# Kernel tuning notes

Measured on AMD Instinct MI355X. Metric: run time of the kernel, lower is better.

The kernel has to match this reference:

```python
import jax, jax.numpy as jnp
import numpy as np

N = 200000   # gaussians
M = 10000    # scaffold nodes
K = 16       # skinning knn
T = 40       # time steps
F = 32       # semantic feature dim
MAX_S = 0.1
MIN_S = 0.0
EPS = 1e-8


def _qnorm(q):
    return q / jnp.clip(jnp.linalg.norm(q, axis=-1, keepdims=True), 1e-12)


def q2R(q):
    # quaternion (w, x, y, z) -> rotation matrix, normalizing first (matches q2R in source)
    q = _qnorm(q)
    w, x, y, z = q[..., 0], q[..., 1], q[..., 2], q[..., 3]
    r0 = jnp.stack([1 - 2 * (y * y + z * z), 2 * (x * y - w * z), 2 * (x * z + w * y)], -1)
    r1 = jnp.stack([2 * (x * y + w * z), 1 - 2 * (x * x + z * z), 2 * (y * z - w * x)], -1)
    r2 = jnp.stack([2 * (x * z - w * y), 2 * (y * z + w * x), 1 - 2 * (x * x + y * y)], -1)
    return jnp.stack([r0, r1, r2], -2)


def quat_mul(a, b):
    aw, ax, ay, az = a[..., 0], a[..., 1], a[..., 2], a[..., 3]
    bw, bx, by, bz = b[..., 0], b[..., 1], b[..., 2], b[..., 3]
    return jnp.stack([
        aw * bw - ax * bx - ay * by - az * bz,
        aw * bx + ax * bw + ay * bz - az * by,
        aw * by - ax * bz + ay * bw + az * bx,
        aw * bz + ax * by - ay * bx + az * bw], -1)


def quat_conj(q):
    return q * jnp.array([1.0, -1.0, -1.0, -1.0], q.dtype)


def setup_inputs() -> dict:
    key = jax.random.key(0)
    ks = jax.random.split(key, 13)
    return {
        "gs_xyz": 0.05 * jax.random.normal(ks[0], (N, 3), jnp.float32),
        "gs_rotation": jax.random.normal(ks[1], (N, 4), jnp.float32),
        "gs_scaling": jax.random.normal(ks[2], (N, 3), jnp.float32),
        "gs_opacity": jax.random.normal(ks[3], (N, 1), jnp.float32),
        "feat_dc": jax.random.normal(ks[4], (N, 3), jnp.float32),
        "feat_rest": jax.random.normal(ks[5], (N, 9), jnp.float32),
        "node_xyz": jax.random.normal(ks[6], (T, M, 3), jnp.float32),
        "node_quat": jax.random.normal(ks[7], (T, M, 4), jnp.float32),
        "node_sigma": 0.1 + 0.5 * jax.random.uniform(ks[8], (M, 1), jnp.float32),
        "node_sem": jax.random.normal(ks[9], (M, F), jnp.float32),
        "attach_ind": jax.random.randint(ks[10], (N,), 0, M, jnp.int32),
        "ref_time": jax.random.randint(ks[11], (N,), 0, T, jnp.int32),
        "topo_knn": jax.random.randint(ks[12], (M, K), 0, M, jnp.int32),
        "t": 5,
    }


def reference(gs_xyz, gs_rotation, gs_scaling, gs_opacity, feat_dc, feat_rest,
              node_xyz, node_quat, node_sigma, node_sem,
              attach_ind, ref_time, topo_knn, t):
    # --- per-gaussian activated attributes ---
    s = MIN_S + jax.nn.sigmoid(gs_scaling) * (MAX_S - MIN_S)   # s_act
    o = jax.nn.sigmoid(gs_opacity)                              # o_act
    sph = jnp.concatenate([feat_dc, feat_rest], axis=-1)        # [N, 12], full sph order

    # --- leaf-local -> world at ref time (get_xyz / get_R_mtx) ---
    ref_p_attach = node_xyz[ref_time, attach_ind]               # [N,3] async knn gather
    ref_q_attach = node_quat[ref_time, attach_ind]              # [N,4]
    R_ref_attach = q2R(ref_q_attach)                            # [N,3,3]
    x_world = jnp.einsum('nij,nj->ni', R_ref_attach, gs_xyz) + ref_p_attach
    R_world = jnp.einsum('nij,njk->nik', R_ref_attach, q2R(gs_rotation))

    # --- scf.warp: KNN skinning from per-point ref time to target time t ---
    sk_ind = topo_knn[attach_ind]                               # [N,K] neighbor node ids
    p_ref = node_xyz[ref_time[:, None], sk_ind]                 # [N,K,3]
    q_ref = node_quat[ref_time[:, None], sk_ind]                # [N,K,4]
    p_live = node_xyz[t][sk_ind]                                # [N,K,3]
    q_live = node_quat[t][sk_ind]                               # [N,K,4]
    sigma = node_sigma[sk_ind, 0]                               # [N,K]

    diff = x_world[:, None, :] - p_ref                          # [N,K,3]
    dsq = jnp.sum(diff * diff, axis=-1)                         # [N,K]
    w = jnp.exp(-dsq / (2.0 * sigma * sigma + EPS))             # RBF skinning weights
    w = w / (jnp.sum(w, axis=-1, keepdims=True) + EPS)          # [N,K]

    # per-node relative transform ref -> live
    q_rel = quat_mul(_qnorm(q_live), quat_conj(_qnorm(q_ref)))  # [N,K,4]
    R_rel = q2R(q_rel)                                          # [N,K,3,3]
    mu_k = jnp.einsum('nkij,nkj->nki', R_rel, diff) + p_live    # [N,K,3]
    mu_live = jnp.einsum('nk,nki->ni', w, mu_k)                 # [N,3]

    q_blend = jnp.einsum('nk,nkd->nd', w, q_rel)                # blended quaternion
    fr_live = jnp.einsum('nij,njk->nik', q2R(q_blend), R_world) # [N,3,3]

    sem_live = jnp.einsum('nk,nkf->nf', w, node_sem[sk_ind])    # [N,F]

    return mu_live, fr_live, s, o, sph, sem_live
```

## Files before the change

### kernel.cpp

```cpp
#include <hip/hip_runtime.h>

#define KNN 16
#define FSEM 32
#define LPG 4

__device__ __forceinline__ float sigmoidf_(float x) { return 1.0f / (1.0f + __expf(-x)); }

__device__ __forceinline__ void quat_to_R(float qw, float qx, float qy, float qz, float* R) {
    float d = qw * qw + qx * qx + qy * qy + qz * qz;
    float inv = rsqrtf(fmaxf(d, 1e-24f));
    float w = qw * inv, x = qx * inv, y = qy * inv, z = qz * inv;
    R[0] = 1.f - 2.f * (y * y + z * z); R[1] = 2.f * (x * y - w * z); R[2] = 2.f * (x * z + w * y);
    R[3] = 2.f * (x * y + w * z); R[4] = 1.f - 2.f * (x * x + z * z); R[5] = 2.f * (y * z - w * x);
    R[6] = 2.f * (x * z - w * y); R[7] = 2.f * (y * z + w * x); R[8] = 1.f - 2.f * (x * x + y * y);
}

__global__ void __launch_bounds__(256)
k_pack(const float* __restrict__ node_xyz, const float* __restrict__ node_quat,
       float* __restrict__ packed, int TM)
{
    int p = blockIdx.x * blockDim.x + threadIdx.x;
    if (p >= TM) return;
    const float* x = node_xyz + 3 * (size_t)p;
    float4 a = make_float4(x[0], x[1], x[2], 0.f);
    float4 q = reinterpret_cast<const float4*>(node_quat)[p];
    float4* dst = reinterpret_cast<float4*>(packed + 8 * (size_t)p);
    dst[0] = a;
    dst[1] = q;
}

template<bool FR>
__global__ void __launch_bounds__(256)
k_elem(const float* __restrict__ gs_scal,
       const float* __restrict__ gs_opa,
       const float* __restrict__ feat_dc,
       const float* __restrict__ feat_rest,
       const float* __restrict__ gs_rot,
       const float* __restrict__ node_quat,
       const int*   __restrict__ attach_ind,
       const int*   __restrict__ ref_time,
       const float* __restrict__ qb_ws,
       float* __restrict__ out, int N, int M)
{
    const int n = blockIdx.x * blockDim.x + threadIdx.x;
    if (n >= N) return;
    const size_t Ns = (size_t)N, ns = (size_t)n;

    float* os = out + 12 * Ns + 3 * ns;
    os[0] = 0.1f * sigmoidf_(gs_scal[3 * ns + 0]);
    os[1] = 0.1f * sigmoidf_(gs_scal[3 * ns + 1]);
    os[2] = 0.1f * sigmoidf_(gs_scal[3 * ns + 2]);

    out[15 * Ns + ns] = sigmoidf_(gs_opa[ns]);

    float* osph = out + 16 * Ns + 12 * ns;
    float4 v0 = make_float4(feat_dc[3 * ns + 0], feat_dc[3 * ns + 1], feat_dc[3 * ns + 2],
                            feat_rest[9 * ns + 0]);
    float4 v1 = make_float4(feat_rest[9 * ns + 1], feat_rest[9 * ns + 2],
                            feat_rest[9 * ns + 3], feat_rest[9 * ns + 4]);
    float4 v2 = make_float4(feat_rest[9 * ns + 5], feat_rest[9 * ns + 6],
                            feat_rest[9 * ns + 7], feat_rest[9 * ns + 8]);
    reinterpret_cast<float4*>(osph)[0] = v0;
    reinterpret_cast<float4*>(osph)[1] = v1;
    reinterpret_cast<float4*>(osph)[2] = v2;

    if constexpr (FR) {
        const int a  = attach_ind[n];
        const int rt = ref_time[n];
        const float4 qa = reinterpret_cast<const float4*>(node_quat)[(size_t)rt * (size_t)M + (size_t)a];
        float Rref[9];
        quat_to_R(qa.x, qa.y, qa.z, qa.w, Rref);

        const float4 qg = reinterpret_cast<const float4*>(gs_rot)[ns];
        float Rg[9];
        quat_to_R(qg.x, qg.y, qg.z, qg.w, Rg);

        float Rw[9];
#pragma unroll
        for (int i = 0; i < 3; i++)
#pragma unroll
            for (int j = 0; j < 3; j++)
                Rw[3 * i + j] = Rref[3 * i] * Rg[j] + Rref[3 * i + 1] * Rg[3 + j] + Rref[3 * i + 2] * Rg[6 + j];

        const float4 qb = reinterpret_cast<const float4*>(qb_ws)[ns];
        float Rb[9];
        quat_to_R(qb.x, qb.y, qb.z, qb.w, Rb);

        float* ofr = out + 3 * Ns + 9 * ns;
#pragma unroll
        for (int i = 0; i < 3; i++)
#pragma unroll
            for (int j = 0; j < 3; j++)
                ofr[3 * i + j] = Rb[3 * i] * Rw[j] + Rb[3 * i + 1] * Rw[3 + j] + Rb[3 * i + 2] * Rw[6 + j];
    }
}

template<bool PACKED, bool FRSPLIT>
__global__ void __launch_bounds__(256)
dynscf_kernel(const float* __restrict__ gs_xyz,
              const float* __restrict__ gs_rot,
              const float* __restrict__ node_xyz,
              const float* __restrict__ node_quat,
              const float* __restrict__ packed,
              const float* __restrict__ node_sigma,
              const float* __restrict__ node_sem,
              const int* __restrict__ attach_ind,
              const int* __restrict__ ref_time,
              const int* __restrict__ topo_knn,
              const int* __restrict__ t_ptr,
              float* __restrict__ out,
              float* __restrict__ qb_out,
              int N, int M)
{
    const int tid = blockIdx.x * blockDim.x + threadIdx.x;
    const int n   = tid >> 2;
    const int sub = tid & (LPG - 1);
    if (n >= N) return;

    const int t  = t_ptr[0];
    const int a  = attach_ind[n];
    const int rt = ref_time[n];

    const size_t base_rt = (size_t)rt * (size_t)M;
    const size_t base_t  = (size_t)t  * (size_t)M;

    const int4 kv = reinterpret_cast<const int4*>(topo_knn)[(size_t)a * (KNN / 4) + sub];
    const int js[4] = { kv.x, kv.y, kv.z, kv.w };

    float apx, apy, apz, aqw, aqx, aqy, aqz;
    if (PACKED) {
        const float4* pk = reinterpret_cast<const float4*>(packed + (base_rt + (size_t)a) * 8);
        float4 xz = pk[0], qv = pk[1];
        apx = xz.x; apy = xz.y; apz = xz.z;
        aqw = qv.x; aqx = qv.y; aqy = qv.z; aqz = qv.w;
    } else {
        const float4 qv = *reinterpret_cast<const float4*>(node_quat + (base_rt + (size_t)a) * 4);
        const float* pa = node_xyz + (base_rt + (size_t)a) * 3;
        apx = pa[0]; apy = pa[1]; apz = pa[2];
        aqw = qv.x; aqx = qv.y; aqy = qv.z; aqz = qv.w;
    }
    float Rref[9];
    quat_to_R(aqw, aqx, aqy, aqz, Rref);

    const float gx = gs_xyz[3 * (size_t)n + 0];
    const float gy = gs_xyz[3 * (size_t)n + 1];
    const float gz = gs_xyz[3 * (size_t)n + 2];

    const float xw0 = Rref[0] * gx + Rref[1] * gy + Rref[2] * gz + apx;
    const float xw1 = Rref[3] * gx + Rref[4] * gy + Rref[5] * gz + apy;
    const float xw2 = Rref[6] * gx + Rref[7] * gy + Rref[8] * gz + apz;

    float wsum = 0.f, mu0 = 0.f, mu1 = 0.f, mu2 = 0.f;
    float qb0 = 0.f, qb1 = 0.f, qb2 = 0.f, qb3 = 0.f;
    float wk[4];

#pragma unroll
    for (int k = 0; k < KNN / LPG; k++) {
        const int j = js[k];

        float prx, pry, prz, rw, rx, ry, rz;
        float plx, ply, plz, lw, lx, ly, lz;
        if (PACKED) {
            const float4* pkr = reinterpret_cast<const float4*>(packed + (base_rt + (size_t)j) * 8);
            float4 xr = pkr[0], qr = pkr[1];
            prx = xr.x; pry = xr.y; prz = xr.z;
            rw = qr.x; rx = qr.y; ry = qr.z; rz = qr.w;
            const float4* pkl = reinterpret_cast<const float4*>(packed + (base_t + (size_t)j) * 8);
            float4 xl = pkl[0], ql = pkl[1];
            plx = xl.x; ply = xl.y; plz = xl.z;
            lw = ql.x; lx = ql.y; ly = ql.z; lz = ql.w;
        } else {
            const float* pr = node_xyz + (base_rt + (size_t)j) * 3;
            prx = pr[0]; pry = pr[1]; prz = pr[2];
            const float4 qr = *reinterpret_cast<const float4*>(node_quat + (base_rt + (size_t)j) * 4);
            rw = qr.x; rx = qr.y; ry = qr.z; rz = qr.w;
            const float* pl = node_xyz + (base_t + (size_t)j) * 3;
            plx = pl[0]; ply = pl[1]; plz = pl[2];
            const float4 ql = *reinterpret_cast<const float4*>(node_quat + (base_t + (size_t)j) * 4);
            lw = ql.x; lx = ql.y; ly = ql.z; lz = ql.w;
        }

        const float dx = xw0 - prx;
        const float dy = xw1 - pry;
        const float dz = xw2 - prz;
        const float dsq = dx * dx + dy * dy + dz * dz;

        const float sg = node_sigma[j];
        const float w = __expf(-dsq / (2.f * sg * sg + 1e-8f));
        wk[k] = w;

        {
            float inv = rsqrtf(fmaxf(rw * rw + rx * rx + ry * ry + rz * rz, 1e-24f));
            rw *= inv; rx *= inv; ry *= inv; rz *= inv;
        }
        {
            float inv = rsqrtf(fmaxf(lw * lw + lx * lx + ly * ly + lz * lz, 1e-24f));
            lw *= inv; lx *= inv; ly *= inv; lz *= inv;
        }
        const float qw =  lw * rw + lx * rx + ly * ry + lz * rz;
        const float qx = -lw * rx + lx * rw - ly * rz + lz * ry;
        const float qy = -lw * ry + lx * rz + ly * rw - lz * rx;
        const float qz = -lw * rz - lx * ry + ly * rx + lz * rw;

        float Rr[9];
        quat_to_R(qw, qx, qy, qz, Rr);

        const float m0 = Rr[0] * dx + Rr[1] * dy + Rr[2] * dz + plx;
        const float m1 = Rr[3] * dx + Rr[4] * dy + Rr[5] * dz + ply;
        const float m2 = Rr[6] * dx + Rr[7] * dy + Rr[8] * dz + plz;

        wsum += w;
        mu0 += w * m0; mu1 += w * m1; mu2 += w * m2;
        qb0 += w * qw; qb1 += w * qx; qb2 += w * qy; qb3 += w * qz;
    }

#pragma unroll
    for (int m = 1; m < LPG; m <<= 1) {
        wsum += __shfl_xor(wsum, m);
        mu0  += __shfl_xor(mu0, m);  mu1 += __shfl_xor(mu1, m);  mu2 += __shfl_xor(mu2, m);
        qb0  += __shfl_xor(qb0, m);  qb1 += __shfl_xor(qb1, m);
        qb2  += __shfl_xor(qb2, m);  qb3 += __shfl_xor(qb3, m);
    }

    const float invw = 1.f / (wsum + 1e-8f);
    const size_t Ns = (size_t)N, ns = (size_t)n;

    float sm0 = 0.f, sm1 = 0.f, sm2 = 0.f, sm3 = 0.f;
    float sm4 = 0.f, sm5 = 0.f, sm6 = 0.f, sm7 = 0.f;
    const float4* sem4 = reinterpret_cast<const float4*>(node_sem);
#pragma unroll
    for (int kk = 0; kk < KNN; kk++) {
        const int src = kk >> 2;
        const int idx = kk & 3;
        const int   jk = __shfl(js[idx], src, LPG);
        const float wkk = __shfl(wk[idx], src, LPG);
        const float4 v0 = sem4[(size_t)jk * (FSEM / 4) + sub * 2 + 0];
        const float4 v1 = sem4[(size_t)jk * (FSEM / 4) + sub * 2 + 1];
        sm0 += wkk * v0.x; sm1 += wkk * v0.y; sm2 += wkk * v0.z; sm3 += wkk * v0.w;
        sm4 += wkk * v1.x; sm5 += wkk * v1.y; sm6 += wkk * v1.z; sm7 += wkk * v1.w;
    }

    if (sub == 0) {
        out[3 * ns + 0] = mu0 * invw;
        out[3 * ns + 1] = mu1 * invw;
        out[3 * ns + 2] = mu2 * invw;
    } else if (sub == 1) {
        if (FRSPLIT) {
            reinterpret_cast<float4*>(qb_out)[ns] =
                make_float4(qb0 * invw, qb1 * invw, qb2 * invw, qb3 * invw);
        }
    }

    if constexpr (!FRSPLIT) {
        if (sub == 1) {
            const float4 qg = *reinterpret_cast<const float4*>(gs_rot + 4 * ns);
            float Rg[9];
            quat_to_R(qg.x, qg.y, qg.z, qg.w, Rg);
            float Rw[9];
#pragma unroll
            for (int i = 0; i < 3; i++)
#pragma unroll
                for (int j = 0; j < 3; j++)
                    Rw[3 * i + j] = Rref[3 * i] * Rg[j] + Rref[3 * i + 1] * Rg[3 + j] + Rref[3 * i + 2] * Rg[6 + j];
            float Rb[9];
            quat_to_R(qb0 * invw, qb1 * invw, qb2 * invw, qb3 * invw, Rb);
            float* ofr = out + 3 * Ns + 9 * ns;
#pragma unroll
            for (int i = 0; i < 3; i++)
#pragma unroll
                for (int j = 0; j < 3; j++)
                    ofr[3 * i + j] = Rb[3 * i] * Rw[j] + Rb[3 * i + 1] * Rw[3 + j] + Rb[3 * i + 2] * Rw[6 + j];
        }
    }

    float4* osem = reinterpret_cast<float4*>(out + 28 * Ns + FSEM * ns);
    osem[sub * 2 + 0] = make_float4(sm0 * invw, sm1 * invw, sm2 * invw, sm3 * invw);
    osem[sub * 2 + 1] = make_float4(sm4 * invw, sm5 * invw, sm6 * invw, sm7 * invw);
}

extern "C" void kernel_launch(void* const* d_in, const int* in_sizes, int n_in,
                              void* d_out, int out_size, void* d_ws, size_t ws_size,
                              hipStream_t stream)
{
    const float* gs_xyz     = (const float*)d_in[0];
    const float* gs_rot     = (const float*)d_in[1];
    const float* gs_scal    = (const float*)d_in[2];
    const float* gs_opa     = (const float*)d_in[3];
    const float* feat_dc    = (const float*)d_in[4];
    const float* feat_rest  = (const float*)d_in[5];
    const float* node_xyz   = (const float*)d_in[6];
    const float* node_quat  = (const float*)d_in[7];
    const float* node_sigma = (const float*)d_in[8];
    const float* node_sem   = (const float*)d_in[9];
    const int* attach_ind   = (const int*)d_in[10];
    const int* ref_time     = (const int*)d_in[11];
    const int* topo_knn     = (const int*)d_in[12];
    const int* t_ptr        = (const int*)d_in[13];

    const int N = in_sizes[0] / 3;
    const int M = in_sizes[8];
    const int TM = in_sizes[6] / 3;

    float* out = (float*)d_out;

    const int block = 256;
    const int gridN = (N + block - 1) / block;
    const long long threads = (long long)N * LPG;
    const int gridM = (int)((threads + block - 1) / block);
    const int gridP = (TM + block - 1) / block;

    const size_t need_packed = (size_t)TM * 8 * sizeof(float);
    const size_t need_qb     = (size_t)N * 4 * sizeof(float);

    if (ws_size >= need_packed + need_qb) {
        float* packed = (float*)d_ws;
        float* qb_ws  = (float*)d_ws + (size_t)TM * 8;
        hipLaunchKernelGGL(k_pack, dim3(gridP), dim3(block), 0, stream,
                           node_xyz, node_quat, packed, TM);
        hipLaunchKernelGGL((dynscf_kernel<true, true>), dim3(gridM), dim3(block), 0, stream,
                           gs_xyz, gs_rot, node_xyz, node_quat, packed, node_sigma, node_sem,
                           attach_ind, ref_time, topo_knn, t_ptr, out, qb_ws, N, M);
        hipLaunchKernelGGL((k_elem<true>), dim3(gridN), dim3(block), 0, stream,
                           gs_scal, gs_opa, feat_dc, feat_rest, gs_rot, node_quat,
                           attach_ind, ref_time, qb_ws, out, N, M);
    } else if (ws_size >= need_qb) {
        float* qb_ws = (float*)d_ws;
        hipLaunchKernelGGL((dynscf_kernel<false, true>), dim3(gridM), dim3(block), 0, stream,
                           gs_xyz, gs_rot, node_xyz, node_quat, (const float*)nullptr,
                           node_sigma, node_sem,
                           attach_ind, ref_time, topo_knn, t_ptr, out, qb_ws, N, M);
        hipLaunchKernelGGL((k_elem<true>), dim3(gridN), dim3(block), 0, stream,
                           gs_scal, gs_opa, feat_dc, feat_rest, gs_rot, node_quat,
                           attach_ind, ref_time, qb_ws, out, N, M);
    } else {
        hipLaunchKernelGGL((dynscf_kernel<false, false>), dim3(gridM), dim3(block), 0, stream,
                           gs_xyz, gs_rot, node_xyz, node_quat, (const float*)nullptr,
                           node_sigma, node_sem,
                           attach_ind, ref_time, topo_knn, t_ptr, out, (float*)nullptr, N, M);
        hipLaunchKernelGGL((k_elem<false>), dim3(gridN), dim3(block), 0, stream,
                           gs_scal, gs_opa, feat_dc, feat_rest, gs_rot, node_quat,
                           attach_ind, ref_time, (const float*)nullptr, out, N, M);
    }
}
```

Baseline: 223.5 us.

## Counting-sort gaussians by (ref_time, attach) key and remap blocks per XCD

Adds a histogram, two-level scan and scatter pass that reorder gaussians by their (ref_time, attach node) key into a packed meta buffer holding index and position. The main skinning kernel then walks gaussians in sorted order, with an XCD-aware block remap, so neighbouring threads gather the same node records and cache reuse improves. Sigma is also folded into the spare lane of the packed node record, which removes a separate gather. The cost is several extra small launches, atomics and scatter traffic, and output writes that are now indexed by the original gaussian and so land out of order.

```diff
diff --git a/kernel.cpp b/kernel.cpp
--- a/kernel.cpp
+++ b/kernel.cpp
@@ -3,6 +3,7 @@
 #define KNN 16
 #define FSEM 32
 #define LPG 4
+#define NXCD 8
 
 __device__ __forceinline__ float sigmoidf_(float x) { return 1.0f / (1.0f + __expf(-x)); }
 
@@ -17,16 +18,97 @@
 
 __global__ void __launch_bounds__(256)
 k_pack(const float* __restrict__ node_xyz, const float* __restrict__ node_quat,
-       float* __restrict__ packed, int TM)
+       const float* __restrict__ node_sigma,
+       float* __restrict__ packed, int* __restrict__ cnt, int TM, int M, int B)
 {
     int p = blockIdx.x * blockDim.x + threadIdx.x;
+    if (p < B && cnt) cnt[p] = 0;
     if (p >= TM) return;
+    const int node = p - (p / M) * M;
     const float* x = node_xyz + 3 * (size_t)p;
-    float4 a = make_float4(x[0], x[1], x[2], 0.f);
+    float4 a = make_float4(x[0], x[1], x[2], node_sigma[node]);
     float4 q = reinterpret_cast<const float4*>(node_quat)[p];
     float4* dst = reinterpret_cast<float4*>(packed + 8 * (size_t)p);
     dst[0] = a;
     dst[1] = q;
+}
+
+__global__ void __launch_bounds__(256)
+k_hist(const int* __restrict__ attach, const int* __restrict__ rtime,
+       int* __restrict__ cnt, int* __restrict__ rank, int N, int M)
+{
+    int n = blockIdx.x * blockDim.x + threadIdx.x;
+    if (n >= N) return;
+    const int key = rtime[n] * M + attach[n];
+    rank[n] = atomicAdd(&cnt[key], 1);
+}
+
+__global__ void __launch_bounds__(256)
+k_scan1(int* __restrict__ cnt, int* __restrict__ blk, int B)
+{
+    __shared__ int sh[256];
+    const int i = blockIdx.x * 256 + threadIdx.x;
+    int v = (i < B) ? cnt[i] : 0;
+    sh[threadIdx.x] = v;
+    __syncthreads();
+    int acc = v;
+#pragma unroll
+    for (int off = 1; off < 256; off <<= 1) {
+        int u = (threadIdx.x >= off) ? sh[threadIdx.x - off] : 0;
+        __syncthreads();
+        acc += u;
+        sh[threadIdx.x] = acc;
+        __syncthreads();
+    }
+    if (i < B) cnt[i] = acc - v;
+    if (threadIdx.x == 255) blk[blockIdx.x] = acc;
+}
+
+__global__ void __launch_bounds__(256)
+k_scan2(int* __restrict__ blk, int nblk)
+{
+    __shared__ int sh[256];
+    __shared__ int carry_s;
+    if (threadIdx.x == 0) carry_s = 0;
+    __syncthreads();
+    for (int base = 0; base < nblk; base += 256) {
+        const int i = base + threadIdx.x;
+        int v = (i < nblk) ? blk[i] : 0;
+        sh[threadIdx.x] = v;
+        __syncthreads();
+        int acc = v;
+#pragma unroll
+        for (int off = 1; off < 256; off <<= 1) {
+            int u = (threadIdx.x >= off) ? sh[threadIdx.x - off] : 0;
+            __syncthreads();
+            acc += u;
+            sh[threadIdx.x] = acc;
+            __syncthreads();
+        }
+        const int carry = carry_s;
+        if (i < nblk) blk[i] = acc - v + carry;
+        __syncthreads();
+        if (threadIdx.x == 255) carry_s = carry + acc;
+        __syncthreads();
+    }
+}
+
+__global__ void __launch_bounds__(256)
+k_scatter(const int* __restrict__ attach, const int* __restrict__ rtime,
+          const float* __restrict__ gs_xyz,
+          const int* __restrict__ rank, const int* __restrict__ cnt,
+          const int* __restrict__ blk, float4* __restrict__ meta, int N, int M)
+{
+    int n = blockIdx.x * blockDim.x + threadIdx.x;
+    if (n >= N) return;
+    const int a = attach[n], rt = rtime[n];
+    const int key = rt * M + a;
+    const int pos = cnt[key] + blk[key >> 8] + rank[n];
+    meta[2 * (size_t)pos]     = make_float4(__int_as_float(n), __int_as_float(a),
+                                            __int_as_float(rt), 0.f);
+    meta[2 * (size_t)pos + 1] = make_float4(gs_xyz[3 * (size_t)n + 0],
+                                            gs_xyz[3 * (size_t)n + 1],
+                                            gs_xyz[3 * (size_t)n + 2], 0.f);
 }
 
 template<bool FR>
@@ -95,7 +177,7 @@
     }
 }
 
-template<bool PACKED, bool FRSPLIT>
+template<bool PACKED, bool FRSPLIT, bool SORTED>
 __global__ void __launch_bounds__(256)
 dynscf_kernel(const float* __restrict__ gs_xyz,
               const float* __restrict__ gs_rot,
@@ -108,18 +190,42 @@
               const int* __restrict__ ref_time,
               const int* __restrict__ topo_knn,
               const int* __restrict__ t_ptr,
+              const float4* __restrict__ meta,
               float* __restrict__ out,
               float* __restrict__ qb_out,
               int N, int M)
 {
-    const int tid = blockIdx.x * blockDim.x + threadIdx.x;
-    const int n   = tid >> 2;
+    int bid = blockIdx.x;
+    if (SORTED) {
+        const int nwg = gridDim.x;
+        const int q = nwg / NXCD, r = nwg % NXCD;
+        const int xcd = bid % NXCD, idx = bid / NXCD;
+        bid = (xcd < r ? xcd * (q + 1) : r * (q + 1) + (xcd - r) * q) + idx;
+    }
+    const int tid = bid * blockDim.x + threadIdx.x;
+    const int g   = tid >> 2;
     const int sub = tid & (LPG - 1);
-    if (n >= N) return;
-
-    const int t  = t_ptr[0];
-    const int a  = attach_ind[n];
-    const int rt = ref_time[n];
+    if (g >= N) return;
+
+    const int t = t_ptr[0];
+
+    int n, a, rt;
+    float gx, gy, gz;
+    if (SORTED) {
+        const float4 m0 = meta[2 * (size_t)g];
+        const float4 m1 = meta[2 * (size_t)g + 1];
+        n  = __float_as_int(m0.x);
+        a  = __float_as_int(m0.y);
+        rt = __float_as_int(m0.z);
+        gx = m1.x; gy = m1.y; gz = m1.z;
+    } else {
+        n  = g;
+        a  = attach_ind[n];
+        rt = ref_time[n];
+        gx = gs_xyz[3 * (size_t)n + 0];
+        gy = gs_xyz[3 * (size_t)n + 1];
+        gz = gs_xyz[3 * (size_t)n + 2];
+    }
 
     const size_t base_rt = (size_t)rt * (size_t)M;
     const size_t base_t  = (size_t)t  * (size_t)M;
@@ -142,10 +248,6 @@
     float Rref[9];
     quat_to_R(aqw, aqx, aqy, aqz, Rref);
 
-    const float gx = gs_xyz[3 * (size_t)n + 0];
-    const float gy = gs_xyz[3 * (size_t)n + 1];
-    const float gz = gs_xyz[3 * (size_t)n + 2];
-
     const float xw0 = Rref[0] * gx + Rref[1] * gy + Rref[2] * gz + apx;
     const float xw1 = Rref[3] * gx + Rref[4] * gy + Rref[5] * gz + apy;
     const float xw2 = Rref[6] * gx + Rref[7] * gy + Rref[8] * gz + apz;
@@ -160,10 +262,11 @@
 
         float prx, pry, prz, rw, rx, ry, rz;
         float plx, ply, plz, lw, lx, ly, lz;
+        float sg;
         if (PACKED) {
             const float4* pkr = reinterpret_cast<const float4*>(packed + (base_rt + (size_t)j) * 8);
             float4 xr = pkr[0], qr = pkr[1];
-            prx = xr.x; pry = xr.y; prz = xr.z;
+            prx = xr.x; pry = xr.y; prz = xr.z; sg = xr.w;
             rw = qr.x; rx = qr.y; ry = qr.z; rz = qr.w;
             const float4* pkl = reinterpret_cast<const float4*>(packed + (base_t + (size_t)j) * 8);
             float4 xl = pkl[0], ql = pkl[1];
@@ -178,6 +281,7 @@
             plx = pl[0]; ply = pl[1]; plz = pl[2];
             const float4 ql = *reinterpret_cast<const float4*>(node_quat + (base_t + (size_t)j) * 4);
             lw = ql.x; lx = ql.y; ly = ql.z; lz = ql.w;
+            sg = node_sigma[j];
         }
 
         const float dx = xw0 - prx;
@@ -185,7 +289,6 @@
         const float dz = xw2 - prz;
         const float dsq = dx * dx + dy * dy + dz * dz;
 
-        const float sg = node_sigma[j];
         const float w = __expf(-dsq / (2.f * sg * sg + 1e-8f));
         wk[k] = w;
 
@@ -300,6 +403,7 @@
     const int N = in_sizes[0] / 3;
     const int M = in_sizes[8];
     const int TM = in_sizes[6] / 3;
+    const int B  = TM;
 
     float* out = (float*)d_out;
 
@@ -308,35 +412,69 @@
     const long long threads = (long long)N * LPG;
     const int gridM = (int)((threads + block - 1) / block);
     const int gridP = (TM + block - 1) / block;
-
-    const size_t need_packed = (size_t)TM * 8 * sizeof(float);
-    const size_t need_qb     = (size_t)N * 4 * sizeof(float);
-
-    if (ws_size >= need_packed + need_qb) {
+    const int nblkS = (B + 255) / 256;
+
+    const size_t f_packed = (size_t)TM * 8;
+    const size_t f_qb     = (size_t)N * 4;
+    const size_t f_meta   = (size_t)N * 8;
+    const size_t i_cnt    = (size_t)B;
+    const size_t i_blk    = 4096;
+    const size_t need_sort   = (f_packed + f_qb + f_meta + i_cnt + i_blk) * sizeof(float);
+    const size_t need_packed = (f_packed + f_qb) * sizeof(float);
+    const size_t need_qb     = f_qb * sizeof(float);
+
+    if (ws_size >= need_sort && nblkS <= 4096) {
+        float*  packed = (float*)d_ws;
+        float*  qb_ws  = packed + f_packed;
+        float4* meta   = (float4*)(packed + f_packed + f_qb);
+        int*    cnt    = (int*)(packed + f_packed + f_qb + f_meta);
+        int*    blk    = cnt + i_cnt;
+        int*    rank   = (int*)qb_ws;
+
+        hipLaunchKernelGGL(k_pack, dim3(gridP), dim3(block), 0, stream,
+                           node_xyz, node_quat, node_sigma, packed, cnt, TM, M, B);
+        hipLaunchKernelGGL(k_hist, dim3(gridN), dim3(block), 0, stream,
+                           attach_ind, ref_time, cnt, rank, N, M);
+        hipLaunchKernelGGL(k_scan1, dim3(nblkS), dim3(block), 0, stream,
+                           cnt, blk, B);
+        hipLaunchKernelGGL(k_scan2, dim3(1), dim3(block), 0, stream,
+                           blk, nblkS);
+        hipLaunchKernelGGL(k_scatter, dim3(gridN), dim3(block), 0, stream,
+                           attach_ind, ref_time, gs_xyz, rank, cnt, blk, meta, N, M);
+        hipLaunchKernelGGL((dynscf_kernel<true, true, true>), dim3(gridM), dim3(block), 0, stream,
+                           gs_xyz, gs_rot, node_xyz, node_quat, packed, node_sigma, node_sem,
+                           attach_ind, ref_time, topo_knn, t_ptr, meta, out, qb_ws, N, M);
+        hipLaunchKernelGGL((k_elem<true>), dim3(gridN), dim3(block), 0, stream,
+                           gs_scal, gs_opa, feat_dc, feat_rest, gs_rot, node_quat,
+                           attach_ind, ref_time, qb_ws, out, N, M);
+    } else if (ws_size >= need_packed) {
         float* packed = (float*)d_ws;
-        float* qb_ws  = (float*)d_ws + (size_t)TM * 8;
+        float* qb_ws  = packed + f_packed;
         hipLaunchKernelGGL(k_pack, dim3(gridP), dim3(block), 0, stream,
-                           node_xyz, node_quat, packed, TM);
-        hipLaunchKernelGGL((dynscf_kernel<true, true>), dim3(gridM), dim3(block), 0, stream,
+                           node_xyz, node_quat, node_sigma, packed, (int*)nullptr, TM, M, 0);
+        hipLaunchKernelGGL((dynscf_kernel<true, true, false>), dim3(gridM), dim3(block), 0, stream,
                            gs_xyz, gs_rot, node_xyz, node_quat, packed, node_sigma, node_sem,
-                           attach_ind, ref_time, topo_knn, t_ptr, out, qb_ws, N, M);
+                           attach_ind, ref_time, topo_knn, t_ptr, (const float4*)nullptr,
+                           out, qb_ws, N, M);
         hipLaunchKernelGGL((k_elem<true>), dim3(gridN), dim3(block), 0, stream,
                            gs_scal, gs_opa, feat_dc, feat_rest, gs_rot, node_quat,
                            attach_ind, ref_time, qb_ws, out, N, M);
     } else if (ws_size >= need_qb) {
         float* qb_ws = (float*)d_ws;
-        hipLaunchKernelGGL((dynscf_kernel<false, true>), dim3(gridM), dim3(block), 0, stream,
+        hipLaunchKernelGGL((dynscf_kernel<false, true, false>), dim3(gridM), dim3(block), 0, stream,
                            gs_xyz, gs_rot, node_xyz, node_quat, (const float*)nullptr,
                            node_sigma, node_sem,
-                           attach_ind, ref_time, topo_knn, t_ptr, out, qb_ws, N, M);
+                           attach_ind, ref_time, topo_knn, t_ptr, (const float4*)nullptr,
+                           out, qb_ws, N, M);
         hipLaunchKernelGGL((k_elem<true>), dim3(gridN), dim3(block), 0, stream,
                            gs_scal, gs_opa, feat_dc, feat_rest, gs_rot, node_quat,
                            attach_ind, ref_time, qb_ws, out, N, M);
     } else {
-        hipLaunchKernelGGL((dynscf_kernel<false, false>), dim3(gridM), dim3(block), 0, stream,
+        hipLaunchKernelGGL((dynscf_kernel<false, false, false>), dim3(gridM), dim3(block), 0, stream,
                            gs_xyz, gs_rot, node_xyz, node_quat, (const float*)nullptr,
                            node_sigma, node_sem,
-                           attach_ind, ref_time, topo_knn, t_ptr, out, (float*)nullptr, N, M);
+                           attach_ind, ref_time, topo_knn, t_ptr, (const float4*)nullptr,
+                           out, (float*)nullptr, N, M);
         hipLaunchKernelGGL((k_elem<false>), dim3(gridN), dim3(block), 0, stream,
                            gs_scal, gs_opa, feat_dc, feat_rest, gs_rot, node_quat,
                            attach_ind, ref_time, (const float*)nullptr, out, N, M);
```

Result: faster. 215.5 us (-3.5%).
